# Performance work log

Hardware: AMD Instinct MI355X
Metric: run time of the kernel (lower is better)

Reference implementation:

```python
import jax, jax.numpy as jnp
import numpy as np

N = 8192
E = 262144
IN_DIM, HID, LAT = 256, 256, 128


def _sage_conv(x, src, dst, W_l, b_l, W_r, n_nodes):
    # PyG SAGEConv (mean aggr): out = lin_l(mean_{j in N(i)} x_j) + lin_r(x_i)
    agg = jax.ops.segment_sum(x[src], dst, num_segments=n_nodes)          # [N, F]
    cnt = jax.ops.segment_sum(jnp.ones((src.shape[0],), x.dtype), dst,
                              num_segments=n_nodes)                       # [N]
    mean = agg / jnp.maximum(cnt, 1.0)[:, None]
    return mean @ W_l + b_l + x @ W_r


def setup_inputs() -> dict:
    key = jax.random.key(0)
    ks = jax.random.split(key, 10)
    s = lambda fin: 1.0 / np.sqrt(fin)
    u = lambda k, shape, fin: jax.random.uniform(k, shape, jnp.float32, -s(fin), s(fin))
    inp = {
        "x": jax.random.normal(ks[0], (N, IN_DIM), jnp.float32),
        "edge_index": jax.random.randint(ks[1], (2, E), 0, N, jnp.int64),
        # conv1: in -> hid
        "W_l1": u(ks[2], (IN_DIM, HID), IN_DIM), "b_l1": u(ks[3], (HID,), IN_DIM),
        "W_r1": u(ks[4], (IN_DIM, HID), IN_DIM),
        # conv2 (mu): hid -> lat
        "W_l2": u(ks[5], (HID, LAT), HID), "b_l2": u(ks[6], (LAT,), HID),
        "W_r2": u(ks[7], (HID, LAT), HID),
        # conv3 (logvar): hid -> lat
        "W_l3": u(ks[8], (HID, LAT), HID), "b_l3": jnp.zeros((LAT,), jnp.float32),
        "W_r3": u(ks[9], (HID, LAT), HID),
    }
    return inp


def reference(x, edge_index, W_l1, b_l1, W_r1, W_l2, b_l2, W_r2, W_l3, b_l3, W_r3):
    src, dst = edge_index[0], edge_index[1]
    h = jax.nn.relu(_sage_conv(x, src, dst, W_l1, b_l1, W_r1, N))
    mu = _sage_conv(h, src, dst, W_l2, b_l2, W_r2, N)
    logvar = _sage_conv(h, src, dst, W_l3, b_l3, W_r3, N)
    # reparameterize
    std = jnp.exp(0.5 * logvar)
    eps = jax.random.normal(jax.random.key(42), std.shape, std.dtype)
    z = mu + eps * std
    # inner-product decode on L2-normalized z
    norm_z = z / (jnp.linalg.norm(z, axis=1, keepdims=True) + 1e-8)
    recon_x = norm_z @ norm_z.T                                           # [N, N]
    return recon_x, mu, logvar, z
```

## Files before the change

kernel.cpp:

```cpp
#include <hip/hip_runtime.h>
#include <hip/hip_bf16.h>

#define NN 8192
#define EE 262144
#define IND 256
#define HIDD 256
#define LATD 128
#define CAP 128

typedef __attribute__((ext_vector_type(8))) short bf16x8;
typedef __attribute__((ext_vector_type(4))) float f32x4;

__device__ __forceinline__ unsigned short bf16u(float f) {
    __hip_bfloat16 h = __float2bfloat16(f);
    return *reinterpret_cast<unsigned short*>(&h);
}

__global__ __launch_bounds__(256) void prep_k(
        const float* __restrict__ x, __hip_bfloat16* __restrict__ x_b,
        const float* __restrict__ Wl1, const float* __restrict__ Wr1,
        const float* __restrict__ Wl2, const float* __restrict__ Wr2,
        const float* __restrict__ Wl3, const float* __restrict__ Wr3,
        __hip_bfloat16* __restrict__ Wl1T, __hip_bfloat16* __restrict__ Wr1T,
        __hip_bfloat16* __restrict__ Wl2T, __hip_bfloat16* __restrict__ Wr2T,
        __hip_bfloat16* __restrict__ Wl3T, __hip_bfloat16* __restrict__ Wr3T,
        int* __restrict__ cur) {
    int gid = blockIdx.x * 256 + threadIdx.x;
    if (gid < NN) cur[gid] = 0;
    if (gid < 524288) {
        f32x4 v = reinterpret_cast<const f32x4*>(x)[gid];
        uint2 o;
        o.x = (unsigned)bf16u(v[0]) | ((unsigned)bf16u(v[1]) << 16);
        o.y = (unsigned)bf16u(v[2]) | ((unsigned)bf16u(v[3]) << 16);
        reinterpret_cast<uint2*>(x_b)[gid] = o;
    } else {
        int g2 = gid - 524288;
        if (g2 < 131072) {
            int i = g2 & 65535;
            const float* W = (g2 < 65536) ? Wl1 : Wr1;
            __hip_bfloat16* Wt = (g2 < 65536) ? Wl1T : Wr1T;
            int k = i >> 8, n = i & 255;
            Wt[n * 256 + k] = __float2bfloat16(W[i]);
        } else {
            int g3 = g2 - 131072;
            int w = g3 >> 15, i = g3 & 32767;
            const float* Ws[4] = {Wl2, Wr2, Wl3, Wr3};
            __hip_bfloat16* Wts[4] = {Wl2T, Wr2T, Wl3T, Wr3T};
            int k = i >> 7, n = i & 127;
            Wts[w][n * 256 + k] = __float2bfloat16(Ws[w][i]);
        }
    }
}

__global__ void fill_adj_k(const int* __restrict__ ei, int* __restrict__ cur,
                           int* __restrict__ adj) {
    int e = blockIdx.x * 256 + threadIdx.x;
    if (e < EE) {
        int d = ei[EE + e];
        int p = atomicAdd(&cur[d], 1);
        adj[(d << 7) + p] = ei[e];
    }
}

__global__ __launch_bounds__(256) void agg_mean4_k(
        const __hip_bfloat16* __restrict__ in, const int* __restrict__ adj,
        const int* __restrict__ deg_a, __hip_bfloat16* __restrict__ out) {
    int node = blockIdx.x * 4 + (threadIdx.x >> 6);
    int lane = threadIdx.x & 63;
    const uint2* inu = (const uint2*)in;
    int deg = deg_a[node];
    int s = node << 7;
    int e = s + deg;
    float a0 = 0.f, a1 = 0.f, a2 = 0.f, a3 = 0.f;
    int j = s;
    for (; j + 4 <= e; j += 4) {
        int n0 = adj[j], n1 = adj[j + 1], n2 = adj[j + 2], n3 = adj[j + 3];
        uint2 u0 = inu[(size_t)n0 * 64 + lane];
        uint2 u1 = inu[(size_t)n1 * 64 + lane];
        uint2 u2 = inu[(size_t)n2 * 64 + lane];
        uint2 u3 = inu[(size_t)n3 * 64 + lane];
        a0 += __uint_as_float(u0.x << 16);
        a1 += __uint_as_float(u0.x & 0xffff0000u);
        a2 += __uint_as_float(u0.y << 16);
        a3 += __uint_as_float(u0.y & 0xffff0000u);
        a0 += __uint_as_float(u1.x << 16);
        a1 += __uint_as_float(u1.x & 0xffff0000u);
        a2 += __uint_as_float(u1.y << 16);
        a3 += __uint_as_float(u1.y & 0xffff0000u);
        a0 += __uint_as_float(u2.x << 16);
        a1 += __uint_as_float(u2.x & 0xffff0000u);
        a2 += __uint_as_float(u2.y << 16);
        a3 += __uint_as_float(u2.y & 0xffff0000u);
        a0 += __uint_as_float(u3.x << 16);
        a1 += __uint_as_float(u3.x & 0xffff0000u);
        a2 += __uint_as_float(u3.y << 16);
        a3 += __uint_as_float(u3.y & 0xffff0000u);
    }
    for (; j < e; ++j) {
        uint2 u = inu[(size_t)adj[j] * 64 + lane];
        a0 += __uint_as_float(u.x << 16);
        a1 += __uint_as_float(u.x & 0xffff0000u);
        a2 += __uint_as_float(u.y << 16);
        a3 += __uint_as_float(u.y & 0xffff0000u);
    }
    float w = 1.0f / (float)max(deg, 1);
    uint2 o;
    o.x = (unsigned)bf16u(a0 * w) | ((unsigned)bf16u(a1 * w) << 16);
    o.y = (unsigned)bf16u(a2 * w) | ((unsigned)bf16u(a3 * w) << 16);
    ((uint2*)out)[(size_t)node * 64 + lane] = o;
}

__global__ __launch_bounds__(256) void conv1_k(
        const __hip_bfloat16* __restrict__ A1, const __hip_bfloat16* __restrict__ Bt1,
        const __hip_bfloat16* __restrict__ A2, const __hip_bfloat16* __restrict__ Bt2,
        const float* __restrict__ bias, __hip_bfloat16* __restrict__ outB) {
    int tid = threadIdx.x;
    int wid = tid >> 6, lane = tid & 63;
    int wm = wid >> 1, wn = wid & 1;
    int row0 = blockIdx.x * 128 + wm * 64;
    int col0 = blockIdx.y * 128 + wn * 64;
    int lrow = lane & 15;
    int lk = (lane >> 4) * 8;

    f32x4 acc[4][4] = {};

#pragma unroll
    for (int p = 0; p < 2; ++p) {
        const __hip_bfloat16* A = (p == 0) ? A1 : A2;
        const __hip_bfloat16* Bt = (p == 0) ? Bt1 : Bt2;
        for (int ks = 0; ks < IND; ks += 32) {
            bf16x8 a[4], b[4];
#pragma unroll
            for (int i = 0; i < 4; ++i)
                a[i] = *reinterpret_cast<const bf16x8*>(
                    A + (size_t)(row0 + i * 16 + lrow) * IND + ks + lk);
#pragma unroll
            for (int i = 0; i < 4; ++i)
                b[i] = *reinterpret_cast<const bf16x8*>(
                    Bt + (size_t)(col0 + i * 16 + lrow) * IND + ks + lk);
#pragma unroll
            for (int mi = 0; mi < 4; ++mi)
#pragma unroll
                for (int ni = 0; ni < 4; ++ni)
                    acc[mi][ni] = __builtin_amdgcn_mfma_f32_16x16x32_bf16(
                        a[mi], b[ni], acc[mi][ni], 0, 0, 0);
        }
    }

    int crow = (lane >> 4) * 4;
    int ccol = lane & 15;
#pragma unroll
    for (int mi = 0; mi < 4; ++mi)
#pragma unroll
        for (int ni = 0; ni < 4; ++ni) {
            int col = col0 + ni * 16 + ccol;
            float badd = bias[col];
#pragma unroll
            for (int j = 0; j < 4; ++j) {
                int row = row0 + mi * 16 + crow + j;
                float v = fmaxf(acc[mi][ni][j] + badd, 0.f);
                outB[(size_t)row * HIDD + col] = __float2bfloat16(v);
            }
        }
}

__global__ __launch_bounds__(256) void conv23_k(
        const __hip_bfloat16* __restrict__ meanh, const __hip_bfloat16* __restrict__ h_b,
        const __hip_bfloat16* __restrict__ Wl2T, const __hip_bfloat16* __restrict__ Wr2T,
        const float* __restrict__ bl2,
        const __hip_bfloat16* __restrict__ Wl3T, const __hip_bfloat16* __restrict__ Wr3T,
        const float* __restrict__ bl3,
        float* __restrict__ muF, __hip_bfloat16* __restrict__ muB,
        float* __restrict__ lvF, __hip_bfloat16* __restrict__ lvB) {
    bool is3 = blockIdx.y != 0;
    const __hip_bfloat16* WlT = is3 ? Wl3T : Wl2T;
    const __hip_bfloat16* WrT = is3 ? Wr3T : Wr2T;
    const float* bias = is3 ? bl3 : bl2;
    float* oF = is3 ? lvF : muF;
    __hip_bfloat16* oB = is3 ? lvB : muB;

    int tid = threadIdx.x;
    int wid = tid >> 6, lane = tid & 63;
    int wm = wid >> 1, wn = wid & 1;
    int row0 = blockIdx.x * 128 + wm * 64;
    int col0 = wn * 64;
    int lrow = lane & 15;
    int lk = (lane >> 4) * 8;

    f32x4 acc[4][4] = {};

#pragma unroll
    for (int p = 0; p < 2; ++p) {
        const __hip_bfloat16* A = (p == 0) ? meanh : h_b;
        const __hip_bfloat16* Bt = (p == 0) ? WlT : WrT;
        for (int ks = 0; ks < HIDD; ks += 32) {
            bf16x8 a[4], b[4];
#pragma unroll
            for (int i = 0; i < 4; ++i)
                a[i] = *reinterpret_cast<const bf16x8*>(
                    A + (size_t)(row0 + i * 16 + lrow) * HIDD + ks + lk);
#pragma unroll
            for (int i = 0; i < 4; ++i)
                b[i] = *reinterpret_cast<const bf16x8*>(
                    Bt + (size_t)(col0 + i * 16 + lrow) * HIDD + ks + lk);
#pragma unroll
            for (int mi = 0; mi < 4; ++mi)
#pragma unroll
                for (int ni = 0; ni < 4; ++ni)
                    acc[mi][ni] = __builtin_amdgcn_mfma_f32_16x16x32_bf16(
                        a[mi], b[ni], acc[mi][ni], 0, 0, 0);
        }
    }

    int crow = (lane >> 4) * 4;
    int ccol = lane & 15;
#pragma unroll
    for (int mi = 0; mi < 4; ++mi)
#pragma unroll
        for (int ni = 0; ni < 4; ++ni) {
            int col = col0 + ni * 16 + ccol;
            float badd = bias[col];
#pragma unroll
            for (int j = 0; j < 4; ++j) {
                int row = row0 + mi * 16 + crow + j;
                float v = acc[mi][ni][j] + badd;
                size_t idx = (size_t)row * LATD + col;
                oF[idx] = v;
                oB[idx] = __float2bfloat16(v);
            }
        }
}

__device__ __forceinline__ unsigned rotl32(unsigned x, int r) {
    return (x << r) | (x >> (32 - r));
}

#define TF_ROUND(r)        \
    {                      \
        x0 += x1;          \
        x1 = rotl32(x1, r);\
        x1 ^= x0;          \
    }

__device__ __forceinline__ float tf_normal(unsigned i) {
    const unsigned ks0 = 0u, ks1 = 42u, ks2 = 0u ^ 42u ^ 0x1BD11BDAu;
    unsigned x0 = 0u + ks0;
    unsigned x1 = i + ks1;
    TF_ROUND(13) TF_ROUND(15) TF_ROUND(26) TF_ROUND(6)
    x0 += ks1; x1 += ks2 + 1u;
    TF_ROUND(17) TF_ROUND(29) TF_ROUND(16) TF_ROUND(24)
    x0 += ks2; x1 += ks0 + 2u;
    TF_ROUND(13) TF_ROUND(15) TF_ROUND(26) TF_ROUND(6)
    x0 += ks0; x1 += ks1 + 3u;
    TF_ROUND(17) TF_ROUND(29) TF_ROUND(16) TF_ROUND(24)
    x0 += ks1; x1 += ks2 + 4u;
    TF_ROUND(13) TF_ROUND(15) TF_ROUND(26) TF_ROUND(6)
    x0 += ks2; x1 += ks0 + 5u;
    unsigned bits = x0 ^ x1;
    float f = __uint_as_float((bits >> 9) | 0x3f800000u) - 1.0f;
    const float lo = -0.99999994f;
    float u = fmaxf(f * 2.0f + lo, lo);
    return 1.41421356f * erfinvf(u);
}

__global__ void reparam_norm_k(const __hip_bfloat16* __restrict__ mu_b,
                               const __hip_bfloat16* __restrict__ lv_b,
                               float* __restrict__ z_out, __hip_bfloat16* __restrict__ nz) {
    int row = blockIdx.x;
    int t = threadIdx.x;
    size_t b = (size_t)row * LATD;
    int c0 = t, c1 = t + 64;
    float m0 = __bfloat162float(mu_b[b + c0]);
    float m1 = __bfloat162float(mu_b[b + c1]);
    float s0 = expf(0.5f * __bfloat162float(lv_b[b + c0]));
    float s1 = expf(0.5f * __bfloat162float(lv_b[b + c1]));
    float z0 = m0 + tf_normal((unsigned)(b + c0)) * s0;
    float z1 = m1 + tf_normal((unsigned)(b + c1)) * s1;
    float s = z0 * z0 + z1 * z1;
#pragma unroll
    for (int o = 32; o; o >>= 1) s += __shfl_xor(s, o);
    float inv = 1.0f / (sqrtf(s) + 1e-8f);
    z_out[b + c0] = z0;
    z_out[b + c1] = z1;
    nz[b + c0] = __float2bfloat16(z0 * inv);
    nz[b + c1] = __float2bfloat16(z1 * inv);
}

__global__ __launch_bounds__(256) void recon_k(const __hip_bfloat16* __restrict__ nz,
                                               float* __restrict__ out) {
    __shared__ float lds[128][132];
    int tid = threadIdx.x;
    int wid = tid >> 6, lane = tid & 63;
    int wm = wid >> 1, wn = wid & 1;
    int row0 = blockIdx.x * 128 + wm * 64;
    int col0 = blockIdx.y * 128 + wn * 64;
    int lrow = lane & 15;
    int lk = (lane >> 4) * 8;

    f32x4 acc[4][4] = {};

    for (int ks = 0; ks < LATD; ks += 32) {
        bf16x8 a[4], b[4];
#pragma unroll
        for (int i = 0; i < 4; ++i)
            a[i] = *reinterpret_cast<const bf16x8*>(
                nz + (size_t)(row0 + i * 16 + lrow) * LATD + ks + lk);
#pragma unroll
        for (int i = 0; i < 4; ++i)
            b[i] = *reinterpret_cast<const bf16x8*>(
                nz + (size_t)(col0 + i * 16 + lrow) * LATD + ks + lk);
#pragma unroll
        for (int mi = 0; mi < 4; ++mi)
#pragma unroll
            for (int ni = 0; ni < 4; ++ni)
                acc[mi][ni] = __builtin_amdgcn_mfma_f32_16x16x32_bf16(
                    a[mi], b[ni], acc[mi][ni], 0, 0, 0);
    }

    int crow = (lane >> 4) * 4;
    int ccol = lane & 15;
#pragma unroll
    for (int mi = 0; mi < 4; ++mi)
#pragma unroll
        for (int ni = 0; ni < 4; ++ni) {
            int cl = wn * 64 + ni * 16 + ccol;
            int rb = wm * 64 + mi * 16 + crow;
#pragma unroll
            for (int j = 0; j < 4; ++j) lds[rb + j][cl] = acc[mi][ni][j];
        }
    __syncthreads();

    int r = tid >> 5, c4 = tid & 31;
    size_t base = (size_t)(blockIdx.x * 128) * NN + blockIdx.y * 128;
#pragma unroll
    for (int it = 0; it < 16; ++it) {
        int rr = it * 8 + r;
        f32x4 v = *reinterpret_cast<const f32x4*>(&lds[rr][c4 * 4]);
        __builtin_nontemporal_store(
            v, reinterpret_cast<f32x4*>(&out[base + (size_t)rr * NN + c4 * 4]));
    }
}

extern "C" void kernel_launch(void* const* d_in, const int* in_sizes, int n_in,
                              void* d_out, int out_size, void* d_ws, size_t ws_size,
                              hipStream_t stream) {
    const float* x = (const float*)d_in[0];
    const int* ei = (const int*)d_in[1];
    const float* Wl1 = (const float*)d_in[2];
    const float* bl1 = (const float*)d_in[3];
    const float* Wr1 = (const float*)d_in[4];
    const float* Wl2 = (const float*)d_in[5];
    const float* bl2 = (const float*)d_in[6];
    const float* Wr2 = (const float*)d_in[7];
    const float* Wl3 = (const float*)d_in[8];
    const float* bl3 = (const float*)d_in[9];
    const float* Wr3 = (const float*)d_in[10];

    float* out = (float*)d_out;
    char* ws = (char*)d_ws;

    const size_t MU_OFF = (size_t)NN * NN;
    const size_t LV_OFF = MU_OFF + (size_t)NN * LATD;
    const size_t Z_OFF = LV_OFF + (size_t)NN * LATD;

    int* cur = (int*)(ws + 0);
    int* adj = (int*)(ws + 32768);
    __hip_bfloat16* Wl1T = (__hip_bfloat16*)(ws + 4227072);
    __hip_bfloat16* Wr1T = (__hip_bfloat16*)(ws + 4358144);
    __hip_bfloat16* Wl2T = (__hip_bfloat16*)(ws + 4489216);
    __hip_bfloat16* Wr2T = (__hip_bfloat16*)(ws + 4554752);
    __hip_bfloat16* Wl3T = (__hip_bfloat16*)(ws + 4620288);
    __hip_bfloat16* Wr3T = (__hip_bfloat16*)(ws + 4685824);
    __hip_bfloat16* x_b = (__hip_bfloat16*)(ws + 4751360);
    __hip_bfloat16* meanx = (__hip_bfloat16*)(ws + 8945664);
    __hip_bfloat16* mu_b = (__hip_bfloat16*)(ws + 8945664);
    __hip_bfloat16* lv_b = (__hip_bfloat16*)(ws + 11042816);
    __hip_bfloat16* h_b = (__hip_bfloat16*)(ws + 13139968);
    __hip_bfloat16* meanh = (__hip_bfloat16*)(ws + 17334272);
    __hip_bfloat16* nz = (__hip_bfloat16*)(ws + 21528576);

    prep_k<<<3072, 256, 0, stream>>>(x, x_b, Wl1, Wr1, Wl2, Wr2, Wl3, Wr3,
                                     Wl1T, Wr1T, Wl2T, Wr2T, Wl3T, Wr3T, cur);
    fill_adj_k<<<EE / 256, 256, 0, stream>>>(ei, cur, adj);

    agg_mean4_k<<<NN / 4, 256, 0, stream>>>(x_b, adj, cur, meanx);
    conv1_k<<<dim3(NN / 128, HIDD / 128), 256, 0, stream>>>(meanx, Wl1T, x_b, Wr1T, bl1,
                                                            h_b);

    agg_mean4_k<<<NN / 4, 256, 0, stream>>>(h_b, adj, cur, meanh);
    conv23_k<<<dim3(NN / 128, 2), 256, 0, stream>>>(
        meanh, h_b, Wl2T, Wr2T, bl2, Wl3T, Wr3T, bl3,
        out + MU_OFF, mu_b, out + LV_OFF, lv_b);
    reparam_norm_k<<<NN, 64, 0, stream>>>(mu_b, lv_b, out + Z_OFF, nz);

    recon_k<<<dim3(NN / 128, NN / 128), 256, 0, stream>>>(nz, out);
}
```

Before: 181.8 us.

## Fuse pre-decode stages into one cooperative persistent kernel with grid syncs

Replaces the seven kernel launches before the decoder (prep, adjacency fill, two aggregations, two conv GEMMs, reparam) with a single cooperative kernel. Stages are separated by grid.sync and use grid-stride loops over nodes, tiles and rows. This removes per-launch overhead and the gaps between small kernels. In exchange it limits occupancy to co-resident blocks, and each grid barrier and the fixed tile counts (only 128 GEMM tiles) can leave CUs idle. The old multi-kernel path stays as a fallback if the cooperative launch fails.

```diff
diff --git a/kernel.cpp b/kernel.cpp
--- a/kernel.cpp
+++ b/kernel.cpp
@@ -1,5 +1,8 @@
 #include <hip/hip_runtime.h>
 #include <hip/hip_bf16.h>
+#include <hip/hip_cooperative_groups.h>
+
+namespace cg = cooperative_groups;
 
 #define NN 8192
 #define EE 262144
@@ -16,57 +19,43 @@
     return *reinterpret_cast<unsigned short*>(&h);
 }
 
-__global__ __launch_bounds__(256) void prep_k(
-        const float* __restrict__ x, __hip_bfloat16* __restrict__ x_b,
-        const float* __restrict__ Wl1, const float* __restrict__ Wr1,
+
+__device__ __forceinline__ void dev_xconv(int i, const float* __restrict__ x,
+                                          __hip_bfloat16* __restrict__ x_b) {
+    f32x4 v = reinterpret_cast<const f32x4*>(x)[i];
+    uint2 o;
+    o.x = (unsigned)bf16u(v[0]) | ((unsigned)bf16u(v[1]) << 16);
+    o.y = (unsigned)bf16u(v[2]) | ((unsigned)bf16u(v[3]) << 16);
+    reinterpret_cast<uint2*>(x_b)[i] = o;
+}
+
+__device__ __forceinline__ void dev_wtrans(
+        int g2, const float* __restrict__ Wl1, const float* __restrict__ Wr1,
         const float* __restrict__ Wl2, const float* __restrict__ Wr2,
         const float* __restrict__ Wl3, const float* __restrict__ Wr3,
         __hip_bfloat16* __restrict__ Wl1T, __hip_bfloat16* __restrict__ Wr1T,
         __hip_bfloat16* __restrict__ Wl2T, __hip_bfloat16* __restrict__ Wr2T,
-        __hip_bfloat16* __restrict__ Wl3T, __hip_bfloat16* __restrict__ Wr3T,
-        int* __restrict__ cur) {
-    int gid = blockIdx.x * 256 + threadIdx.x;
-    if (gid < NN) cur[gid] = 0;
-    if (gid < 524288) {
-        f32x4 v = reinterpret_cast<const f32x4*>(x)[gid];
-        uint2 o;
-        o.x = (unsigned)bf16u(v[0]) | ((unsigned)bf16u(v[1]) << 16);
-        o.y = (unsigned)bf16u(v[2]) | ((unsigned)bf16u(v[3]) << 16);
-        reinterpret_cast<uint2*>(x_b)[gid] = o;
+        __hip_bfloat16* __restrict__ Wl3T, __hip_bfloat16* __restrict__ Wr3T) {
+    if (g2 < 131072) {
+        int i = g2 & 65535;
+        const float* W = (g2 < 65536) ? Wl1 : Wr1;
+        __hip_bfloat16* Wt = (g2 < 65536) ? Wl1T : Wr1T;
+        int k = i >> 8, n = i & 255;
+        Wt[n * 256 + k] = __float2bfloat16(W[i]);
     } else {
-        int g2 = gid - 524288;
-        if (g2 < 131072) {
-            int i = g2 & 65535;
-            const float* W = (g2 < 65536) ? Wl1 : Wr1;
-            __hip_bfloat16* Wt = (g2 < 65536) ? Wl1T : Wr1T;
-            int k = i >> 8, n = i & 255;
-            Wt[n * 256 + k] = __float2bfloat16(W[i]);
-        } else {
-            int g3 = g2 - 131072;
-            int w = g3 >> 15, i = g3 & 32767;
-            const float* Ws[4] = {Wl2, Wr2, Wl3, Wr3};
-            __hip_bfloat16* Wts[4] = {Wl2T, Wr2T, Wl3T, Wr3T};
-            int k = i >> 7, n = i & 127;
-            Wts[w][n * 256 + k] = __float2bfloat16(Ws[w][i]);
-        }
-    }
-}
-
-__global__ void fill_adj_k(const int* __restrict__ ei, int* __restrict__ cur,
-                           int* __restrict__ adj) {
-    int e = blockIdx.x * 256 + threadIdx.x;
-    if (e < EE) {
-        int d = ei[EE + e];
-        int p = atomicAdd(&cur[d], 1);
-        adj[(d << 7) + p] = ei[e];
-    }
-}
-
-__global__ __launch_bounds__(256) void agg_mean4_k(
-        const __hip_bfloat16* __restrict__ in, const int* __restrict__ adj,
-        const int* __restrict__ deg_a, __hip_bfloat16* __restrict__ out) {
-    int node = blockIdx.x * 4 + (threadIdx.x >> 6);
-    int lane = threadIdx.x & 63;
+        int g3 = g2 - 131072;
+        int w = g3 >> 15, i = g3 & 32767;
+        const float* Ws[4] = {Wl2, Wr2, Wl3, Wr3};
+        __hip_bfloat16* Wts[4] = {Wl2T, Wr2T, Wl3T, Wr3T};
+        int k = i >> 7, n = i & 127;
+        Wts[w][n * 256 + k] = __float2bfloat16(Ws[w][i]);
+    }
+}
+
+__device__ __forceinline__ void dev_agg_node(
+        int node, int lane, const __hip_bfloat16* __restrict__ in,
+        const int* __restrict__ adj, const int* __restrict__ deg_a,
+        __hip_bfloat16* __restrict__ out) {
     const uint2* inu = (const uint2*)in;
     int deg = deg_a[node];
     int s = node << 7;
@@ -110,15 +99,15 @@
     ((uint2*)out)[(size_t)node * 64 + lane] = o;
 }
 
-__global__ __launch_bounds__(256) void conv1_k(
-        const __hip_bfloat16* __restrict__ A1, const __hip_bfloat16* __restrict__ Bt1,
-        const __hip_bfloat16* __restrict__ A2, const __hip_bfloat16* __restrict__ Bt2,
-        const float* __restrict__ bias, __hip_bfloat16* __restrict__ outB) {
-    int tid = threadIdx.x;
+__device__ __forceinline__ void dev_conv1_tile(
+        int bx, int by, int tid, const __hip_bfloat16* __restrict__ A1,
+        const __hip_bfloat16* __restrict__ Bt1, const __hip_bfloat16* __restrict__ A2,
+        const __hip_bfloat16* __restrict__ Bt2, const float* __restrict__ bias,
+        __hip_bfloat16* __restrict__ outB) {
     int wid = tid >> 6, lane = tid & 63;
     int wm = wid >> 1, wn = wid & 1;
-    int row0 = blockIdx.x * 128 + wm * 64;
-    int col0 = blockIdx.y * 128 + wn * 64;
+    int row0 = bx * 128 + wm * 64;
+    int col0 = by * 128 + wn * 64;
     int lrow = lane & 15;
     int lk = (lane >> 4) * 8;
 
@@ -164,25 +153,24 @@
         }
 }
 
-__global__ __launch_bounds__(256) void conv23_k(
-        const __hip_bfloat16* __restrict__ meanh, const __hip_bfloat16* __restrict__ h_b,
+__device__ __forceinline__ void dev_conv23_tile(
+        int bx, int is3, int tid, const __hip_bfloat16* __restrict__ meanh,
+        const __hip_bfloat16* __restrict__ h_b,
         const __hip_bfloat16* __restrict__ Wl2T, const __hip_bfloat16* __restrict__ Wr2T,
         const float* __restrict__ bl2,
         const __hip_bfloat16* __restrict__ Wl3T, const __hip_bfloat16* __restrict__ Wr3T,
-        const float* __restrict__ bl3,
-        float* __restrict__ muF, __hip_bfloat16* __restrict__ muB,
-        float* __restrict__ lvF, __hip_bfloat16* __restrict__ lvB) {
-    bool is3 = blockIdx.y != 0;
+        const float* __restrict__ bl3, float* __restrict__ muF,
+        __hip_bfloat16* __restrict__ muB, float* __restrict__ lvF,
+        __hip_bfloat16* __restrict__ lvB) {
     const __hip_bfloat16* WlT = is3 ? Wl3T : Wl2T;
     const __hip_bfloat16* WrT = is3 ? Wr3T : Wr2T;
     const float* bias = is3 ? bl3 : bl2;
     float* oF = is3 ? lvF : muF;
     __hip_bfloat16* oB = is3 ? lvB : muB;
 
-    int tid = threadIdx.x;
     int wid = tid >> 6, lane = tid & 63;
     int wm = wid >> 1, wn = wid & 1;
-    int row0 = blockIdx.x * 128 + wm * 64;
+    int row0 = bx * 128 + wm * 64;
     int col0 = wn * 64;
     int lrow = lane & 15;
     int lk = (lane >> 4) * 8;
@@ -263,11 +251,10 @@
     return 1.41421356f * erfinvf(u);
 }
 
-__global__ void reparam_norm_k(const __hip_bfloat16* __restrict__ mu_b,
-                               const __hip_bfloat16* __restrict__ lv_b,
-                               float* __restrict__ z_out, __hip_bfloat16* __restrict__ nz) {
-    int row = blockIdx.x;
-    int t = threadIdx.x;
+__device__ __forceinline__ void dev_reparam_row(
+        int row, int t, const __hip_bfloat16* __restrict__ mu_b,
+        const __hip_bfloat16* __restrict__ lv_b, float* __restrict__ z_out,
+        __hip_bfloat16* __restrict__ nz) {
     size_t b = (size_t)row * LATD;
     int c0 = t, c1 = t + 64;
     float m0 = __bfloat162float(mu_b[b + c0]);
@@ -284,6 +271,122 @@
     z_out[b + c1] = z1;
     nz[b + c0] = __float2bfloat16(z0 * inv);
     nz[b + c1] = __float2bfloat16(z1 * inv);
+}
+
+struct FusedParams {
+    const float* x;
+    const int* ei;
+    const float *Wl1, *bl1, *Wr1, *Wl2, *bl2, *Wr2, *Wl3, *bl3, *Wr3;
+    __hip_bfloat16 *x_b, *Wl1T, *Wr1T, *Wl2T, *Wr2T, *Wl3T, *Wr3T;
+    int *cur, *adj;
+    __hip_bfloat16 *meanx, *h_b, *meanh, *mu_b, *lv_b, *nz;
+    float *muF, *lvF, *zF;
+};
+
+__global__ __launch_bounds__(256) void fused_k(FusedParams p) {
+    cg::grid_group grid = cg::this_grid();
+    const int tid = threadIdx.x;
+    const int gid = blockIdx.x * 256 + tid;
+    const int stride = gridDim.x * 256;
+    const int wave = blockIdx.x * 4 + (tid >> 6);
+    const int nwaves = gridDim.x * 4;
+    const int lane = tid & 63;
+
+    for (int i = gid; i < NN; i += stride) p.cur[i] = 0;
+    for (int i = gid; i < 524288; i += stride) dev_xconv(i, p.x, p.x_b);
+    for (int i = gid; i < 262144; i += stride)
+        dev_wtrans(i, p.Wl1, p.Wr1, p.Wl2, p.Wr2, p.Wl3, p.Wr3, p.Wl1T, p.Wr1T,
+                   p.Wl2T, p.Wr2T, p.Wl3T, p.Wr3T);
+    grid.sync();
+
+    for (int e = gid; e < EE; e += stride) {
+        int d = p.ei[EE + e];
+        int pos = atomicAdd(&p.cur[d], 1);
+        p.adj[(d << 7) + pos] = p.ei[e];
+    }
+    grid.sync();
+
+    for (int node = wave; node < NN; node += nwaves)
+        dev_agg_node(node, lane, p.x_b, p.adj, p.cur, p.meanx);
+    grid.sync();
+
+    for (int t = blockIdx.x; t < 128; t += gridDim.x)
+        dev_conv1_tile(t >> 1, t & 1, tid, p.meanx, p.Wl1T, p.x_b, p.Wr1T, p.bl1,
+                       p.h_b);
+    grid.sync();
+
+    for (int node = wave; node < NN; node += nwaves)
+        dev_agg_node(node, lane, p.h_b, p.adj, p.cur, p.meanh);
+    grid.sync();
+
+    for (int t = blockIdx.x; t < 128; t += gridDim.x)
+        dev_conv23_tile(t >> 1, t & 1, tid, p.meanh, p.h_b, p.Wl2T, p.Wr2T, p.bl2,
+                        p.Wl3T, p.Wr3T, p.bl3, p.muF, p.mu_b, p.lvF, p.lv_b);
+    grid.sync();
+
+    for (int row = wave; row < NN; row += nwaves)
+        dev_reparam_row(row, lane, p.mu_b, p.lv_b, p.zF, p.nz);
+}
+
+__global__ __launch_bounds__(256) void prep_k(
+        const float* __restrict__ x, __hip_bfloat16* __restrict__ x_b,
+        const float* __restrict__ Wl1, const float* __restrict__ Wr1,
+        const float* __restrict__ Wl2, const float* __restrict__ Wr2,
+        const float* __restrict__ Wl3, const float* __restrict__ Wr3,
+        __hip_bfloat16* __restrict__ Wl1T, __hip_bfloat16* __restrict__ Wr1T,
+        __hip_bfloat16* __restrict__ Wl2T, __hip_bfloat16* __restrict__ Wr2T,
+        __hip_bfloat16* __restrict__ Wl3T, __hip_bfloat16* __restrict__ Wr3T,
+        int* __restrict__ cur) {
+    int gid = blockIdx.x * 256 + threadIdx.x;
+    if (gid < NN) cur[gid] = 0;
+    if (gid < 524288) {
+        dev_xconv(gid, x, x_b);
+    } else {
+        dev_wtrans(gid - 524288, Wl1, Wr1, Wl2, Wr2, Wl3, Wr3, Wl1T, Wr1T, Wl2T,
+                   Wr2T, Wl3T, Wr3T);
+    }
+}
+
+__global__ void fill_adj_k(const int* __restrict__ ei, int* __restrict__ cur,
+                           int* __restrict__ adj) {
+    int e = blockIdx.x * 256 + threadIdx.x;
+    if (e < EE) {
+        int d = ei[EE + e];
+        int p = atomicAdd(&cur[d], 1);
+        adj[(d << 7) + p] = ei[e];
+    }
+}
+
+__global__ __launch_bounds__(256) void agg_mean4_k(
+        const __hip_bfloat16* __restrict__ in, const int* __restrict__ adj,
+        const int* __restrict__ deg_a, __hip_bfloat16* __restrict__ out) {
+    int node = blockIdx.x * 4 + (threadIdx.x >> 6);
+    dev_agg_node(node, threadIdx.x & 63, in, adj, deg_a, out);
+}
+
+__global__ __launch_bounds__(256) void conv1_k(
+        const __hip_bfloat16* __restrict__ A1, const __hip_bfloat16* __restrict__ Bt1,
+        const __hip_bfloat16* __restrict__ A2, const __hip_bfloat16* __restrict__ Bt2,
+        const float* __restrict__ bias, __hip_bfloat16* __restrict__ outB) {
+    dev_conv1_tile(blockIdx.x, blockIdx.y, threadIdx.x, A1, Bt1, A2, Bt2, bias, outB);
+}
+
+__global__ __launch_bounds__(256) void conv23_k(
+        const __hip_bfloat16* __restrict__ meanh, const __hip_bfloat16* __restrict__ h_b,
+        const __hip_bfloat16* __restrict__ Wl2T, const __hip_bfloat16* __restrict__ Wr2T,
+        const float* __restrict__ bl2,
+        const __hip_bfloat16* __restrict__ Wl3T, const __hip_bfloat16* __restrict__ Wr3T,
+        const float* __restrict__ bl3,
+        float* __restrict__ muF, __hip_bfloat16* __restrict__ muB,
+        float* __restrict__ lvF, __hip_bfloat16* __restrict__ lvB) {
+    dev_conv23_tile(blockIdx.x, blockIdx.y, threadIdx.x, meanh, h_b, Wl2T, Wr2T, bl2,
+                    Wl3T, Wr3T, bl3, muF, muB, lvF, lvB);
+}
+
+__global__ void reparam_norm_k(const __hip_bfloat16* __restrict__ mu_b,
+                               const __hip_bfloat16* __restrict__ lv_b,
+                               float* __restrict__ z_out, __hip_bfloat16* __restrict__ nz) {
+    dev_reparam_row(blockIdx.x, threadIdx.x, mu_b, lv_b, z_out, nz);
 }
 
 __global__ __launch_bounds__(256) void recon_k(const __hip_bfloat16* __restrict__ nz,
@@ -379,19 +482,43 @@
     __hip_bfloat16* meanh = (__hip_bfloat16*)(ws + 17334272);
     __hip_bfloat16* nz = (__hip_bfloat16*)(ws + 21528576);
 
-    prep_k<<<3072, 256, 0, stream>>>(x, x_b, Wl1, Wr1, Wl2, Wr2, Wl3, Wr3,
-                                     Wl1T, Wr1T, Wl2T, Wr2T, Wl3T, Wr3T, cur);
-    fill_adj_k<<<EE / 256, 256, 0, stream>>>(ei, cur, adj);
-
-    agg_mean4_k<<<NN / 4, 256, 0, stream>>>(x_b, adj, cur, meanx);
-    conv1_k<<<dim3(NN / 128, HIDD / 128), 256, 0, stream>>>(meanx, Wl1T, x_b, Wr1T, bl1,
-                                                            h_b);
-
-    agg_mean4_k<<<NN / 4, 256, 0, stream>>>(h_b, adj, cur, meanh);
-    conv23_k<<<dim3(NN / 128, 2), 256, 0, stream>>>(
-        meanh, h_b, Wl2T, Wr2T, bl2, Wl3T, Wr3T, bl3,
-        out + MU_OFF, mu_b, out + LV_OFF, lv_b);
-    reparam_norm_k<<<NN, 64, 0, stream>>>(mu_b, lv_b, out + Z_OFF, nz);
+    FusedParams prm;
+    prm.x = x; prm.ei = ei;
+    prm.Wl1 = Wl1; prm.bl1 = bl1; prm.Wr1 = Wr1;
+    prm.Wl2 = Wl2; prm.bl2 = bl2; prm.Wr2 = Wr2;
+    prm.Wl3 = Wl3; prm.bl3 = bl3; prm.Wr3 = Wr3;
+    prm.x_b = x_b; prm.Wl1T = Wl1T; prm.Wr1T = Wr1T; prm.Wl2T = Wl2T;
+    prm.Wr2T = Wr2T; prm.Wl3T = Wl3T; prm.Wr3T = Wr3T;
+    prm.cur = cur; prm.adj = adj;
+    prm.meanx = meanx; prm.h_b = h_b; prm.meanh = meanh;
+    prm.mu_b = mu_b; prm.lv_b = lv_b; prm.nz = nz;
+    prm.muF = out + MU_OFF; prm.lvF = out + LV_OFF; prm.zF = out + Z_OFF;
+
+    bool coop_ok = false;
+    int perCU = 0;
+    if (hipOccupancyMaxActiveBlocksPerMultiprocessor(&perCU, fused_k, 256, 0) ==
+            hipSuccess &&
+        perCU > 0) {
+        int G = perCU * 256;
+        if (G > 2048) G = 2048;
+        void* args[] = {(void*)&prm};
+        coop_ok = hipLaunchCooperativeKernel((void*)fused_k, dim3(G), dim3(256), args,
+                                             0, stream) == hipSuccess;
+    }
+
+    if (!coop_ok) {
+        prep_k<<<3072, 256, 0, stream>>>(x, x_b, Wl1, Wr1, Wl2, Wr2, Wl3, Wr3, Wl1T,
+                                         Wr1T, Wl2T, Wr2T, Wl3T, Wr3T, cur);
+        fill_adj_k<<<EE / 256, 256, 0, stream>>>(ei, cur, adj);
+        agg_mean4_k<<<NN / 4, 256, 0, stream>>>(x_b, adj, cur, meanx);
+        conv1_k<<<dim3(NN / 128, HIDD / 128), 256, 0, stream>>>(meanx, Wl1T, x_b, Wr1T,
+                                                                bl1, h_b);
+        agg_mean4_k<<<NN / 4, 256, 0, stream>>>(h_b, adj, cur, meanh);
+        conv23_k<<<dim3(NN / 128, 2), 256, 0, stream>>>(meanh, h_b, Wl2T, Wr2T, bl2,
+                                                        Wl3T, Wr3T, bl3, out + MU_OFF,
+                                                        mu_b, out + LV_OFF, lv_b);
+        reparam_norm_k<<<NN, 64, 0, stream>>>(mu_b, lv_b, out + Z_OFF, nz);
+    }
 
     recon_k<<<dim3(NN / 128, NN / 128), 256, 0, stream>>>(nz, out);
 }
```

Measured after the change: 438.9 us. +141.4%, slower.
